# Kernel optimization log

Hardware: AMD Instinct MI355X
Metric: run time of the kernel (lower is better)

The kernel has to match this reference:

```python
import jax, jax.numpy as jnp
import numpy as np

N_NODES = 100000
HIDDEN = 128
N_EDGES = 1600000


def setup_inputs() -> dict:
    key = jax.random.key(0)
    k_z, k_e, k_w1, k_b1, k_w2, k_b2 = jax.random.split(key, 6)
    z = jax.random.normal(k_z, (N_NODES, HIDDEN), dtype=jnp.float32)
    edge_index = jax.random.randint(k_e, (2, N_EDGES), 0, N_NODES, dtype=jnp.int64)
    # torch.nn.Linear default init: U(-1/sqrt(fan_in), 1/sqrt(fan_in))
    lim1 = 1.0 / np.sqrt(2 * HIDDEN)
    W1 = jax.random.uniform(k_w1, (2 * HIDDEN, HIDDEN), minval=-lim1, maxval=lim1, dtype=jnp.float32)
    b1 = jax.random.uniform(k_b1, (HIDDEN,), minval=-lim1, maxval=lim1, dtype=jnp.float32)
    lim2 = 1.0 / np.sqrt(HIDDEN)
    W2 = jax.random.uniform(k_w2, (HIDDEN, 1), minval=-lim2, maxval=lim2, dtype=jnp.float32)
    b2 = jax.random.uniform(k_b2, (1,), minval=-lim2, maxval=lim2, dtype=jnp.float32)
    return {"z": z, "edge_index": edge_index, "W1": W1, "b1": b1, "W2": W2, "b2": b2}


def reference(z, edge_index, W1, b1, W2, b2):
    src = edge_index[0]
    dst = edge_index[1]
    # gather node pairs -> concat: [E, 2H]
    edge_feat = jnp.concatenate([z[src], z[dst]], axis=1)
    h = jax.nn.relu(edge_feat @ W1 + b1)  # [E, H]
    score = h @ W2 + b2                   # [E, 1]
    return score
```

## Files before the change

### kernel.cpp

```cpp
#include <hip/hip_runtime.h>
#include <hip/hip_bf16.h>
#include <stdint.h>

#define HIDDEN 128

typedef __attribute__((ext_vector_type(8))) short bf16x8;
typedef __attribute__((ext_vector_type(16))) float f32x16;

static __device__ __forceinline__ uint32_t cvt2(float a, float b) {
    union { __hip_bfloat162 h2; uint32_t u; } c;
    c.h2 = __float22bfloat162_rn(make_float2(a, b));
    return c.u;
}
static __device__ __forceinline__ float bf_lo(uint32_t p) {
    union { uint32_t u; float f; } v; v.u = p << 16; return v.f;
}
static __device__ __forceinline__ float bf_hi(uint32_t p) {
    union { uint32_t u; float f; } v; v.u = p & 0xffff0000u; return v.f;
}

__global__ __launch_bounds__(256) void transpose_w1(
    const float* __restrict__ W1, unsigned short* __restrict__ Wt)
{
    const int t = blockIdx.x * 256 + threadIdx.x;
    if (t >= 4096) return;
    const int cc = t >> 4;
    const int kg = t & 15;
    const int ccol = cc & 127;
    const int kofs = (cc >= 128) ? 128 : 0;
    uint32_t u[4];
    #pragma unroll
    for (int p = 0; p < 4; ++p) {
        const float a = W1[(size_t)(kofs + kg * 8 + 2 * p) * 128 + ccol];
        const float b = W1[(size_t)(kofs + kg * 8 + 2 * p + 1) * 128 + ccol];
        u[p] = cvt2(a, b);
    }
    uint4 o = { u[0], u[1], u[2], u[3] };
    *reinterpret_cast<uint4*>(Wt + (size_t)cc * 128 + kg * 8) = o;
}



__global__ __launch_bounds__(256) void precompute_mfma32(
    const float* __restrict__ z, const float* __restrict__ W1,
    const unsigned short* __restrict__ Wt,
    unsigned short* __restrict__ UV, int n_nodes, int n_groups)
{
    __shared__ char Zt[32 * 256];
    __shared__ char Sm[32 * 512];

    const int tid = threadIdx.x;
    const int lane = tid & 63;
    const int w = tid >> 6;
    const int nl = lane & 31;
    const int hi = lane >> 5;

    const int st_node = tid >> 3;
    const int st_j2 = tid & 7;
    const int st_swz = (st_node & 7) << 4;
    const int st_addrA = st_node * 256 + ((st_j2 * 32) ^ st_swz);
    const int st_addrB = st_node * 256 + ((st_j2 * 32 + 16) ^ st_swz);

    bf16x8 wf[2][8];
    if (Wt) {
        #pragma unroll
        for (int cg = 0; cg < 2; ++cg) {
            const int cc = w * 64 + cg * 32 + nl;
            #pragma unroll
            for (int ks = 0; ks < 8; ++ks)
                wf[cg][ks] = *reinterpret_cast<const bf16x8*>(
                    Wt + (size_t)cc * 128 + ks * 16 + hi * 8);
        }
    } else {
        #pragma unroll
        for (int cg = 0; cg < 2; ++cg) {
            const int cc = w * 64 + cg * 32 + nl;
            const int ccol = cc & 127;
            const int kofs = (cc >= 128) ? 128 : 0;
            #pragma unroll
            for (int ks = 0; ks < 8; ++ks) {
                const int k0 = ks * 16 + hi * 8 + kofs;
                float t[8];
                #pragma unroll
                for (int j = 0; j < 8; ++j)
                    t[j] = W1[(size_t)(k0 + j) * 128 + ccol];
                union { uint32_t u[4]; bf16x8 v; } fu;
                fu.u[0] = cvt2(t[0], t[1]); fu.u[1] = cvt2(t[2], t[3]);
                fu.u[2] = cvt2(t[4], t[5]); fu.u[3] = cvt2(t[6], t[7]);
                wf[cg][ks] = fu.v;
            }
        }
    }

    const int stride = gridDim.x;
    int ng = blockIdx.x;
    if (ng >= n_groups) return;

    float4 nz0, nz1, nz2, nz3;
    {
        int node = ng * 32 + st_node;
        node = (node < n_nodes) ? node : (n_nodes - 1);
        const float* zp = z + (size_t)node * HIDDEN + st_j2 * 16;
        nz0 = *reinterpret_cast<const float4*>(zp);
        nz1 = *reinterpret_cast<const float4*>(zp + 4);
        nz2 = *reinterpret_cast<const float4*>(zp + 8);
        nz3 = *reinterpret_cast<const float4*>(zp + 12);
    }

    while (ng < n_groups) {
        {
            uint4 A, B;
            A.x = cvt2(nz0.x, nz0.y); A.y = cvt2(nz0.z, nz0.w);
            A.z = cvt2(nz1.x, nz1.y); A.w = cvt2(nz1.z, nz1.w);
            B.x = cvt2(nz2.x, nz2.y); B.y = cvt2(nz2.z, nz2.w);
            B.z = cvt2(nz3.x, nz3.y); B.w = cvt2(nz3.z, nz3.w);
            *reinterpret_cast<uint4*>(Zt + st_addrA) = A;
            *reinterpret_cast<uint4*>(Zt + st_addrB) = B;
        }

        const int ngn = ng + stride;
        if (ngn < n_groups) {
            int node = ngn * 32 + st_node;
            node = (node < n_nodes) ? node : (n_nodes - 1);
            const float* zp = z + (size_t)node * HIDDEN + st_j2 * 16;
            nz0 = *reinterpret_cast<const float4*>(zp);
            nz1 = *reinterpret_cast<const float4*>(zp + 4);
            nz2 = *reinterpret_cast<const float4*>(zp + 8);
            nz3 = *reinterpret_cast<const float4*>(zp + 12);
        }

        __syncthreads();

        {
            const int rd_swz = (nl & 7) << 4;
            bf16x8 zf[8];
            #pragma unroll
            for (int ks = 0; ks < 8; ++ks) {
                const int off = ks * 32 + hi * 16;
                zf[ks] = *reinterpret_cast<const bf16x8*>(
                    Zt + nl * 256 + (off ^ rd_swz));
            }

            f32x16 acc0 = {};
            f32x16 acc1 = {};
            #pragma unroll
            for (int ks = 0; ks < 8; ++ks) {
                acc0 = __builtin_amdgcn_mfma_f32_32x32x16_bf16(wf[0][ks], zf[ks], acc0, 0, 0, 0);
                acc1 = __builtin_amdgcn_mfma_f32_32x32x16_bf16(wf[1][ks], zf[ks], acc1, 0, 0, 0);
            }

            const int swz = (nl & 15) << 3;
            #pragma unroll
            for (int g = 0; g < 4; ++g) {
                uint2 s0, s1;
                s0.x = cvt2(acc0[4 * g + 0], acc0[4 * g + 1]);
                s0.y = cvt2(acc0[4 * g + 2], acc0[4 * g + 3]);
                s1.x = cvt2(acc1[4 * g + 0], acc1[4 * g + 1]);
                s1.y = cvt2(acc1[4 * g + 2], acc1[4 * g + 3]);
                const int colb0 = w * 128 + g * 16 + hi * 8;
                const int colb1 = w * 128 + 64 + g * 16 + hi * 8;
                *reinterpret_cast<uint2*>(Sm + nl * 512 + (colb0 ^ swz)) = s0;
                *reinterpret_cast<uint2*>(Sm + nl * 512 + (colb1 ^ swz)) = s1;
            }
        }

        __syncthreads();

        {
            const int colb0 = (tid & 31) * 16;
            #pragma unroll
            for (int rep = 0; rep < 4; ++rep) {
                const int node_local = rep * 8 + (tid >> 5);
                const int swz = (node_local & 15) << 3;
                const uint2 g0 = *reinterpret_cast<const uint2*>(Sm + node_local * 512 + ((colb0) ^ swz));
                const uint2 g1 = *reinterpret_cast<const uint2*>(Sm + node_local * 512 + ((colb0 + 8) ^ swz));
                const int node = ng * 32 + node_local;
                if (node < n_nodes) {
                    uint4 o = { g0.x, g0.y, g1.x, g1.y };
                    *reinterpret_cast<uint4*>(UV + (size_t)node * 256 + (tid & 31) * 8) = o;
                }
            }
        }

        ng = ngn;
    }
}

static __device__ __forceinline__ float dot8(uint4 u, uint4 v,
                                             const float* w, const float* bb) {
    const uint32_t up[4] = { u.x, u.y, u.z, u.w };
    const uint32_t vp[4] = { v.x, v.y, v.z, v.w };
    float s = 0.f;
    #pragma unroll
    for (int p = 0; p < 4; ++p) {
        const float h0 = bf_lo(up[p]) + bf_lo(vp[p]) + bb[2 * p];
        const float h1 = bf_hi(up[p]) + bf_hi(vp[p]) + bb[2 * p + 1];
        s = fmaf(fmaxf(h0, 0.f), w[2 * p], s);
        s = fmaf(fmaxf(h1, 0.f), w[2 * p + 1], s);
    }
    return s;
}
static __device__ __forceinline__ float red16(float s) {
    s += __shfl_xor(s, 1, 64); s += __shfl_xor(s, 2, 64);
    s += __shfl_xor(s, 4, 64); s += __shfl_xor(s, 8, 64);
    return s;
}

#define EPG 8

__global__ __launch_bounds__(256, 4) void edge_score(
    const int* __restrict__ ei, const unsigned short* __restrict__ UV,
    const float* __restrict__ b1, const float* __restrict__ W2,
    const float* __restrict__ b2, float* __restrict__ out, int n_edges)
{
    const int g = (blockIdx.x * 256 + threadIdx.x) >> 4;
    const int q = threadIdx.x & 15;
    const int e0 = g * EPG;
    if (e0 >= n_edges) return;

    const float4 w2a = *reinterpret_cast<const float4*>(W2 + q * 8);
    const float4 w2b = *reinterpret_cast<const float4*>(W2 + q * 8 + 4);
    const float wloc[8] = { w2a.x, w2a.y, w2a.z, w2a.w, w2b.x, w2b.y, w2b.z, w2b.w };
    const float4 b1a = *reinterpret_cast<const float4*>(b1 + q * 8);
    const float4 b1b = *reinterpret_cast<const float4*>(b1 + q * 8 + 4);
    const float bb[8] = { b1a.x, b1a.y, b1a.z, b1a.w, b1b.x, b1b.y, b1b.z, b1b.w };
    const float bias = b2[0];

    const char* UVb = (const char*)UV;
    const uint32_t qo = (uint32_t)q * 16u;

    if (e0 + EPG - 1 < n_edges) {
        const int4 sA = *reinterpret_cast<const int4*>(ei + e0);
        const int4 sB = *reinterpret_cast<const int4*>(ei + e0 + 4);
        const int4 dA = *reinterpret_cast<const int4*>(ei + n_edges + e0);
        const int4 dB = *reinterpret_cast<const int4*>(ei + n_edges + e0 + 4);
        const int sidx[EPG] = { sA.x, sA.y, sA.z, sA.w, sB.x, sB.y, sB.z, sB.w };
        const int didx[EPG] = { dA.x, dA.y, dA.z, dA.w, dB.x, dB.y, dB.z, dB.w };

        uint4 u[EPG], v[EPG];
        #pragma unroll
        for (int i = 0; i < EPG; ++i) {
            u[i] = *reinterpret_cast<const uint4*>(UVb + ((uint32_t)sidx[i] * 512u + qo));
            v[i] = *reinterpret_cast<const uint4*>(UVb + ((uint32_t)didx[i] * 512u + 256u + qo));
        }
        __builtin_amdgcn_sched_barrier(0);

        float s[EPG];
        #pragma unroll
        for (int i = 0; i < EPG; ++i) s[i] = dot8(u[i], v[i], wloc, bb);
        #pragma unroll
        for (int i = 0; i < EPG; ++i) s[i] = red16(s[i]) + bias;

        if (q == 0) {
            float4 oA = { s[0], s[1], s[2], s[3] };
            float4 oB = { s[4], s[5], s[6], s[7] };
            *reinterpret_cast<float4*>(out + e0) = oA;
            *reinterpret_cast<float4*>(out + e0 + 4) = oB;
        }
    } else {
        for (int i = 0; i < EPG; ++i) {
            const int e = e0 + i;
            if (e >= n_edges) break;
            const int si = ei[e];
            const int di = ei[n_edges + e];
            const uint4 uu = *reinterpret_cast<const uint4*>(UVb + ((uint32_t)si * 512u + qo));
            const uint4 vv = *reinterpret_cast<const uint4*>(UVb + ((uint32_t)di * 512u + 256u + qo));
            float s = red16(dot8(uu, vv, wloc, bb));
            if (q == 0) out[e] = s + bias;
        }
    }
}

extern "C" void kernel_launch(void* const* d_in, const int* in_sizes, int n_in,
                              void* d_out, int out_size, void* d_ws, size_t ws_size,
                              hipStream_t stream) {
    const float* z  = (const float*)d_in[0];
    const int*   ei = (const int*)d_in[1];
    const float* W1 = (const float*)d_in[2];
    const float* b1 = (const float*)d_in[3];
    const float* W2 = (const float*)d_in[4];
    const float* b2 = (const float*)d_in[5];
    float* out = (float*)d_out;

    const int n_nodes = in_sizes[0] / HIDDEN;
    const int n_edges = in_sizes[1] / 2;

    unsigned short* UV = (unsigned short*)d_ws;
    const size_t uv_bytes = (size_t)n_nodes * 256 * sizeof(unsigned short);

    unsigned short* Wt = nullptr;
    if (ws_size >= uv_bytes + 256 * 128 * sizeof(unsigned short))
        Wt = UV + (size_t)n_nodes * 256;

    if (Wt) transpose_w1<<<16, 256, 0, stream>>>(W1, Wt);

    {
        const int n_groups = (n_nodes + 31) / 32;
        const int g1 = n_groups < 768 ? n_groups : 768;
        precompute_mfma32<<<g1, 256, 0, stream>>>(z, W1, Wt, UV, n_nodes, n_groups);
    }
    {
        const int groups = (n_edges + EPG - 1) / EPG;
        const int blocks = (groups * 16 + 255) / 256;
        edge_score<<<blocks, 256, 0, stream>>>(ei, UV, b1, W2, b2, out, n_edges);
    }
}
```

Baseline: 133.8 us.

## Bucket-sort edges by source node to improve gather locality in edge scoring

Before scoring, edges are counting-sorted into buckets of 32 source nodes using histogram, scan and scatter kernels. Scores are then permuted back to the original edge order. Block indices in edge_score are also remapped so consecutive blocks run on the same XCD. The aim is better cache reuse for the UV gathers. In exchange it adds four extra launches, a memset, atomics and several full passes over the 1.6M edges.

```diff
diff --git a/kernel.cpp b/kernel.cpp
--- a/kernel.cpp
+++ b/kernel.cpp
@@ -3,6 +3,7 @@
 #include <stdint.h>
 
 #define HIDDEN 128
+#define EPG 8
 
 typedef __attribute__((ext_vector_type(8))) short bf16x8;
 typedef __attribute__((ext_vector_type(16))) float f32x16;
@@ -39,8 +40,6 @@
     *reinterpret_cast<uint4*>(Wt + (size_t)cc * 128 + kg * 8) = o;
 }
 
-
-
 __global__ __launch_bounds__(256) void precompute_mfma32(
     const float* __restrict__ z, const float* __restrict__ W1,
     const unsigned short* __restrict__ Wt,
@@ -186,6 +185,72 @@
     }
 }
 
+__global__ __launch_bounds__(256) void hist_kernel(
+    const int* __restrict__ ei, int* __restrict__ cnt, int n_edges)
+{
+    const int e = blockIdx.x * 256 + threadIdx.x;
+    if (e < n_edges) atomicAdd(&cnt[((unsigned)ei[e]) >> 5], 1);
+}
+
+__global__ __launch_bounds__(1024) void scan_bucket(
+    const int* __restrict__ cnt, int* __restrict__ ofs, int nb)
+{
+    __shared__ int s[1024];
+    const int t = threadIdx.x;
+    const int base = t * 4;
+    int v0 = 0, v1 = 0, v2 = 0, v3 = 0;
+    if (base + 0 < nb) v0 = cnt[base + 0];
+    if (base + 1 < nb) v1 = cnt[base + 1];
+    if (base + 2 < nb) v2 = cnt[base + 2];
+    if (base + 3 < nb) v3 = cnt[base + 3];
+    const int tot = v0 + v1 + v2 + v3;
+    s[t] = tot;
+    __syncthreads();
+    for (int d = 1; d < 1024; d <<= 1) {
+        const int x = (t >= d) ? s[t - d] : 0;
+        __syncthreads();
+        s[t] += x;
+        __syncthreads();
+    }
+    int excl = s[t] - tot;
+    if (base + 0 < nb) ofs[base + 0] = excl; excl += v0;
+    if (base + 1 < nb) ofs[base + 1] = excl; excl += v1;
+    if (base + 2 < nb) ofs[base + 2] = excl; excl += v2;
+    if (base + 3 < nb) ofs[base + 3] = excl;
+}
+
+__global__ __launch_bounds__(256) void scatter_kernel(
+    const int* __restrict__ ei, int* __restrict__ ofs,
+    int* __restrict__ ssrc, int* __restrict__ sdst, int* __restrict__ inv,
+    int n_edges)
+{
+    const int e = blockIdx.x * 256 + threadIdx.x;
+    if (e >= n_edges) return;
+    const int s = ei[e];
+    const int d = ei[n_edges + e];
+    const int pos = atomicAdd(&ofs[((unsigned)s) >> 5], 1);
+    ssrc[pos] = s;
+    sdst[pos] = d;
+    inv[e] = pos;
+}
+
+__global__ __launch_bounds__(256) void permute_out(
+    const float* __restrict__ tmp, const int* __restrict__ inv,
+    float* __restrict__ out, int n_edges)
+{
+    const int e0 = (blockIdx.x * 256 + threadIdx.x) * 4;
+    if (e0 + 3 < n_edges) {
+        const int4 iv = *reinterpret_cast<const int4*>(inv + e0);
+        float4 o = { tmp[iv.x], tmp[iv.y], tmp[iv.z], tmp[iv.w] };
+        *reinterpret_cast<float4*>(out + e0) = o;
+    } else {
+        for (int i = 0; i < 4; ++i) {
+            const int e = e0 + i;
+            if (e < n_edges) out[e] = tmp[inv[e]];
+        }
+    }
+}
+
 static __device__ __forceinline__ float dot8(uint4 u, uint4 v,
                                              const float* w, const float* bb) {
     const uint32_t up[4] = { u.x, u.y, u.z, u.w };
@@ -206,14 +271,18 @@
     return s;
 }
 
-#define EPG 8
-
 __global__ __launch_bounds__(256, 4) void edge_score(
-    const int* __restrict__ ei, const unsigned short* __restrict__ UV,
+    const int* __restrict__ srcp, const int* __restrict__ dstp,
+    const unsigned short* __restrict__ UV,
     const float* __restrict__ b1, const float* __restrict__ W2,
-    const float* __restrict__ b2, float* __restrict__ out, int n_edges)
-{
-    const int g = (blockIdx.x * 256 + threadIdx.x) >> 4;
+    const float* __restrict__ b2, float* __restrict__ outp, int n_edges)
+{
+    const int nb = gridDim.x;
+    const int q8 = nb >> 3, r8 = nb & 7;
+    const int x = blockIdx.x & 7, i = blockIdx.x >> 3;
+    const int vb = (x < r8 ? x * (q8 + 1) : r8 * (q8 + 1) + (x - r8) * q8) + i;
+
+    const int g = (vb * 256 + threadIdx.x) >> 4;
     const int q = threadIdx.x & 15;
     const int e0 = g * EPG;
     if (e0 >= n_edges) return;
@@ -230,43 +299,43 @@
     const uint32_t qo = (uint32_t)q * 16u;
 
     if (e0 + EPG - 1 < n_edges) {
-        const int4 sA = *reinterpret_cast<const int4*>(ei + e0);
-        const int4 sB = *reinterpret_cast<const int4*>(ei + e0 + 4);
-        const int4 dA = *reinterpret_cast<const int4*>(ei + n_edges + e0);
-        const int4 dB = *reinterpret_cast<const int4*>(ei + n_edges + e0 + 4);
+        const int4 sA = *reinterpret_cast<const int4*>(srcp + e0);
+        const int4 sB = *reinterpret_cast<const int4*>(srcp + e0 + 4);
+        const int4 dA = *reinterpret_cast<const int4*>(dstp + e0);
+        const int4 dB = *reinterpret_cast<const int4*>(dstp + e0 + 4);
         const int sidx[EPG] = { sA.x, sA.y, sA.z, sA.w, sB.x, sB.y, sB.z, sB.w };
         const int didx[EPG] = { dA.x, dA.y, dA.z, dA.w, dB.x, dB.y, dB.z, dB.w };
 
         uint4 u[EPG], v[EPG];
         #pragma unroll
-        for (int i = 0; i < EPG; ++i) {
-            u[i] = *reinterpret_cast<const uint4*>(UVb + ((uint32_t)sidx[i] * 512u + qo));
-            v[i] = *reinterpret_cast<const uint4*>(UVb + ((uint32_t)didx[i] * 512u + 256u + qo));
+        for (int ii = 0; ii < EPG; ++ii) {
+            u[ii] = *reinterpret_cast<const uint4*>(UVb + ((uint32_t)sidx[ii] * 512u + qo));
+            v[ii] = *reinterpret_cast<const uint4*>(UVb + ((uint32_t)didx[ii] * 512u + 256u + qo));
         }
         __builtin_amdgcn_sched_barrier(0);
 
         float s[EPG];
         #pragma unroll
-        for (int i = 0; i < EPG; ++i) s[i] = dot8(u[i], v[i], wloc, bb);
+        for (int ii = 0; ii < EPG; ++ii) s[ii] = dot8(u[ii], v[ii], wloc, bb);
         #pragma unroll
-        for (int i = 0; i < EPG; ++i) s[i] = red16(s[i]) + bias;
+        for (int ii = 0; ii < EPG; ++ii) s[ii] = red16(s[ii]) + bias;
 
         if (q == 0) {
             float4 oA = { s[0], s[1], s[2], s[3] };
             float4 oB = { s[4], s[5], s[6], s[7] };
-            *reinterpret_cast<float4*>(out + e0) = oA;
-            *reinterpret_cast<float4*>(out + e0 + 4) = oB;
+            *reinterpret_cast<float4*>(outp + e0) = oA;
+            *reinterpret_cast<float4*>(outp + e0 + 4) = oB;
         }
     } else {
-        for (int i = 0; i < EPG; ++i) {
-            const int e = e0 + i;
+        for (int ii = 0; ii < EPG; ++ii) {
+            const int e = e0 + ii;
             if (e >= n_edges) break;
-            const int si = ei[e];
-            const int di = ei[n_edges + e];
+            const int si = srcp[e];
+            const int di = dstp[e];
             const uint4 uu = *reinterpret_cast<const uint4*>(UVb + ((uint32_t)si * 512u + qo));
             const uint4 vv = *reinterpret_cast<const uint4*>(UVb + ((uint32_t)di * 512u + 256u + qo));
             float s = red16(dot8(uu, vv, wloc, bb));
-            if (q == 0) out[e] = s + bias;
+            if (q == 0) outp[e] = s + bias;
         }
     }
 }
@@ -284,24 +353,48 @@
 
     const int n_nodes = in_sizes[0] / HIDDEN;
     const int n_edges = in_sizes[1] / 2;
-
-    unsigned short* UV = (unsigned short*)d_ws;
-    const size_t uv_bytes = (size_t)n_nodes * 256 * sizeof(unsigned short);
-
-    unsigned short* Wt = nullptr;
-    if (ws_size >= uv_bytes + 256 * 128 * sizeof(unsigned short))
-        Wt = UV + (size_t)n_nodes * 256;
-
-    if (Wt) transpose_w1<<<16, 256, 0, stream>>>(W1, Wt);
+    const int n_buckets = (n_nodes + 31) >> 5;
+
+    char* wsp = (char*)d_ws;
+    size_t off = 0;
+    auto alloc = [&](size_t bytes) -> char* {
+        char* p = wsp + off;
+        off = (off + bytes + 255) & ~(size_t)255;
+        return p;
+    };
+    unsigned short* UV = (unsigned short*)alloc((size_t)n_nodes * 256 * 2);
+    unsigned short* Wt = (unsigned short*)alloc(256 * 128 * 2);
+    const size_t base_need = off;
+    int* cnt  = (int*)alloc((size_t)n_buckets * 4);
+    int* ofs  = (int*)alloc((size_t)n_buckets * 4);
+    int* ssrc = (int*)alloc((size_t)n_edges * 4);
+    int* sdst = (int*)alloc((size_t)n_edges * 4);
+    int* inv  = (int*)alloc((size_t)n_edges * 4);
+    float* tmp = (float*)alloc((size_t)n_edges * 4);
+    const bool have_wt   = ws_size >= base_need;
+    const bool do_sort   = (ws_size >= off) && (n_buckets <= 4096);
+
+    if (have_wt) transpose_w1<<<16, 256, 0, stream>>>(W1, have_wt ? Wt : nullptr);
 
     {
         const int n_groups = (n_nodes + 31) / 32;
         const int g1 = n_groups < 768 ? n_groups : 768;
-        precompute_mfma32<<<g1, 256, 0, stream>>>(z, W1, Wt, UV, n_nodes, n_groups);
-    }
-    {
-        const int groups = (n_edges + EPG - 1) / EPG;
-        const int blocks = (groups * 16 + 255) / 256;
-        edge_score<<<blocks, 256, 0, stream>>>(ei, UV, b1, W2, b2, out, n_edges);
-    }
-}
+        precompute_mfma32<<<g1, 256, 0, stream>>>(z, W1, have_wt ? Wt : nullptr,
+                                                  UV, n_nodes, n_groups);
+    }
+
+    const int groups = (n_edges + EPG - 1) / EPG;
+    const int eblocks = (groups * 16 + 255) / 256;
+    const int lblocks = (n_edges + 255) / 256;
+
+    if (do_sort) {
+        hipMemsetAsync(cnt, 0, (size_t)n_buckets * 4, stream);
+        hist_kernel<<<lblocks, 256, 0, stream>>>(ei, cnt, n_edges);
+        scan_bucket<<<1, 1024, 0, stream>>>(cnt, ofs, n_buckets);
+        scatter_kernel<<<lblocks, 256, 0, stream>>>(ei, ofs, ssrc, sdst, inv, n_edges);
+        edge_score<<<eblocks, 256, 0, stream>>>(ssrc, sdst, UV, b1, W2, b2, tmp, n_edges);
+        permute_out<<<(n_edges / 4 + 255) / 256 + 1, 256, 0, stream>>>(tmp, inv, out, n_edges);
+    } else {
+        edge_score<<<eblocks, 256, 0, stream>>>(ei, ei + n_edges, UV, b1, W2, b2, out, n_edges);
+    }
+}
```

New measurement: 381.5 us. 185% more time.
